# Kernel optimization log

Measured on AMD Instinct MI355X. Metric: run time of the kernel, lower is better.

Reference implementation:

```python
import jax, jax.numpy as jnp
import numpy as np


def setup_inputs() -> dict:
    key = jax.random.key(0)
    k1, k2, k3, k4, k5 = jax.random.split(key, 5)
    B, S, E, T = 64, 2048, 256, 100
    h = jax.random.normal(k1, (B, S, E), dtype=jnp.float32)
    theta = jax.random.uniform(k2, (B, T), dtype=jnp.float32)
    w = jax.random.normal(k3, (E, T), dtype=jnp.float32) * 0.05
    v = jax.random.normal(k4, (E, 1), dtype=jnp.float32) * 0.05
    u = jax.random.normal(k5, (E, E), dtype=jnp.float32) * 0.05
    return {"h": h, "theta": theta, "w": w, "v": v, "u": u}


def reference(h, theta, w, v, u):
    # h: [B,S,E], theta: [B,T], w: [E,T], v: [E,1], u: [E,E]
    theta_w = theta @ w.T                      # [B,E]
    h_u = jnp.einsum('bse,ef->bsf', h, u)      # [B,S,E]
    g = jnp.tanh(theta_w[:, None, :] + h_u) @ v  # [B,S,1]
    weight = jax.nn.softmax(g[..., 0], axis=-1)  # [B,S]
    vec = jnp.einsum('bs,bse->be', weight, h)    # [B,E]
    return vec
```

## Files before the change

kernel.cpp:

```cpp
#include <hip/hip_runtime.h>
#include <hip/hip_bf16.h>
#include <math.h>


#define E_DIM 256
#define GM 32
#define NC 8

typedef __bf16 bf16x8 __attribute__((ext_vector_type(8)));
typedef float  f32x4  __attribute__((ext_vector_type(4)));

__device__ __forceinline__ unsigned short f2bf(float x) {
    return __builtin_bit_cast(unsigned short, (__bf16)x);
}

__device__ __forceinline__ float fast_tanh(float x) {
    const float e = __expf(2.0f * x);
    const float r = __builtin_amdgcn_rcpf(e + 1.0f);
    return fmaf(-2.0f, r, 1.0f);
}

__device__ __forceinline__ unsigned sswz(unsigned slot, unsigned row) {
    return (slot & 48u) | ((slot & 15u) ^ (row & 15u));
}

__global__ __launch_bounds__(256) void k_prep(const float* __restrict__ u,
                                              const float* __restrict__ theta,
                                              const float* __restrict__ w,
                                              unsigned short* __restrict__ u_t,
                                              float* __restrict__ tw,
                                              int T) {
    if (blockIdx.x < E_DIM) {
        const int f = blockIdx.x, e = threadIdx.x;
        u_t[(size_t)f * E_DIM + e] = f2bf(u[(size_t)e * E_DIM + f]);
    } else {
        __shared__ float th[128];
        const int b = blockIdx.x - E_DIM;
        const int e = threadIdx.x;
        if (threadIdx.x < T) th[threadIdx.x] = theta[b * T + threadIdx.x];
        __syncthreads();
        float acc = 0.f;
        for (int t = 0; t < T; ++t) acc = fmaf(th[t], w[e * T + t], acc);
        tw[b * E_DIM + e] = acc;
    }
}

__global__ __launch_bounds__(256, 2) void k_fused(const float* __restrict__ h,
                                                  const unsigned short* __restrict__ u_t,
                                                  const float* __restrict__ tw_,
                                                  const float* __restrict__ v,
                                                  float* __restrict__ partial,
                                                  float* __restrict__ pm,
                                                  float* __restrict__ pd,
                                                  int S, int SC) {
    __shared__ float Abuf[2][GM * E_DIM];
    __shared__ float red[4][GM];
    __shared__ float exw[GM];
    __shared__ float pacc[4][E_DIM];

    const int b   = blockIdx.y;
    const int c0  = blockIdx.x * NC;
    const int tid = threadIdx.x;
    const int w   = tid >> 6;
    const int l   = tid & 63;
    const int lg  = l >> 4;
    const int lc  = l & 15;
    const int f0w = w * 64;

#define STAGE(buf, ch)                                                           \
    {                                                                            \
        const char* hb_ = (const char*)(h + ((size_t)b * S + (size_t)(ch) * GM) * E_DIM); \
        _Pragma("unroll")                                                        \
        for (int r = 0; r < 8; ++r) {                                            \
            const int row = r * 4 + w;                                           \
            const unsigned ss = sswz((unsigned)l, (unsigned)row);                \
            __builtin_amdgcn_global_load_lds(                                    \
                (const __attribute__((address_space(1))) void*)(hb_ + (size_t)row * 1024 + ss * 16), \
                (__attribute__((address_space(3))) void*)((char*)Abuf[buf] + r * 4096 + w * 1024), \
                16, 0, 0);                                                       \
        }                                                                        \
    }

    STAGE(0, c0);

    bf16x8 ub[8][4];
#pragma unroll
    for (int kt = 0; kt < 8; ++kt)
#pragma unroll
        for (int n = 0; n < 4; ++n)
            ub[kt][n] = *reinterpret_cast<const bf16x8*>(
                u_t + (size_t)(f0w + n * 16 + lc) * E_DIM + kt * 32 + lg * 8);

    float tw_f[4], v_f[4];
#pragma unroll
    for (int n = 0; n < 4; ++n) {
        const int f = f0w + n * 16 + lc;
        tw_f[n] = tw_[b * E_DIM + f];
        v_f[n]  = v[f];
    }

    __syncthreads();

    for (int c = 0; c < NC; ++c) {
        const int sc  = c0 + c;
        const int cur = c & 1;

        if (c + 1 < NC) STAGE(cur ^ 1, sc + 1);

        const char* A = (const char*)Abuf[cur];
        f32x4 acc[2][4];
#pragma unroll
        for (int m = 0; m < 2; ++m)
#pragma unroll
            for (int n = 0; n < 4; ++n)
                acc[m][n] = (f32x4){0.f, 0.f, 0.f, 0.f};

#pragma unroll
        for (int kt = 0; kt < 8; ++kt) {
            bf16x8 af[2];
#pragma unroll
            for (int m = 0; m < 2; ++m) {
                const unsigned row = (unsigned)(m * 16 + lc);
                const unsigned s0 = sswz((unsigned)(kt * 8 + lg * 2), row);
                const unsigned s1 = sswz((unsigned)(kt * 8 + lg * 2 + 1), row);
                const f32x4 fa0 = *reinterpret_cast<const f32x4*>(A + row * 1024 + s0 * 16);
                const f32x4 fa1 = *reinterpret_cast<const f32x4*>(A + row * 1024 + s1 * 16);
#pragma unroll
                for (int j = 0; j < 4; ++j) {
                    af[m][j]     = (__bf16)fa0[j];
                    af[m][4 + j] = (__bf16)fa1[j];
                }
            }
#pragma unroll
            for (int n = 0; n < 4; ++n) {
                acc[0][n] = __builtin_amdgcn_mfma_f32_16x16x32_bf16(af[0], ub[kt][n], acc[0][n], 0, 0, 0);
                acc[1][n] = __builtin_amdgcn_mfma_f32_16x16x32_bf16(af[1], ub[kt][n], acc[1][n], 0, 0, 0);
            }
        }

        float rs[2][4] = {};
#pragma unroll
        for (int n = 0; n < 4; ++n)
#pragma unroll
            for (int m = 0; m < 2; ++m)
#pragma unroll
                for (int i = 0; i < 4; ++i)
                    rs[m][i] += fast_tanh(acc[m][n][i] + tw_f[n]) * v_f[n];

#pragma unroll
        for (int off = 1; off < 16; off <<= 1)
#pragma unroll
            for (int m = 0; m < 2; ++m)
#pragma unroll
                for (int i = 0; i < 4; ++i)
                    rs[m][i] += __shfl_xor(rs[m][i], off, 64);

        if (lc == 0) {
#pragma unroll
            for (int m = 0; m < 2; ++m)
#pragma unroll
                for (int i = 0; i < 4; ++i)
                    red[w][m * 16 + lg * 4 + i] = rs[m][i];
        }
        __syncthreads();

        if (tid < GM) {
            const float g = red[0][tid] + red[1][tid] + red[2][tid] + red[3][tid];
            float mx = g;
#pragma unroll
            for (int off = 1; off < 32; off <<= 1)
                mx = fmaxf(mx, __shfl_xor(mx, off, 64));
            const float ex = __expf(g - mx);
            float d = ex;
#pragma unroll
            for (int off = 1; off < 32; off <<= 1)
                d += __shfl_xor(d, off, 64);
            exw[tid] = ex;
            if (tid == 0) {
                pm[(size_t)b * SC + sc] = mx;
                pd[(size_t)b * SC + sc] = d;
            }
        }
        __syncthreads();

        f32x4 a4 = (f32x4){0.f, 0.f, 0.f, 0.f};
#pragma unroll
        for (int j = 0; j < 8; ++j) {
            const unsigned row = (unsigned)(w * 8 + j);
            const float ws = exw[row];
            const unsigned ss = sswz((unsigned)l, row);
            const f32x4 hv = *reinterpret_cast<const f32x4*>(A + row * 1024 + ss * 16);
            a4[0] = fmaf(ws, hv[0], a4[0]);
            a4[1] = fmaf(ws, hv[1], a4[1]);
            a4[2] = fmaf(ws, hv[2], a4[2]);
            a4[3] = fmaf(ws, hv[3], a4[3]);
        }
        *reinterpret_cast<f32x4*>(&pacc[w][l * 4]) = a4;
        __syncthreads();

        partial[((size_t)b * SC + sc) * E_DIM + tid] =
            pacc[0][tid] + pacc[1][tid] + pacc[2][tid] + pacc[3][tid];
    }
#undef STAGE
}

__global__ __launch_bounds__(256) void k_combine(const float* __restrict__ partial,
                                                 const float* __restrict__ pm,
                                                 const float* __restrict__ pd,
                                                 float* __restrict__ out,
                                                 int SC) {
    const int b = blockIdx.x, t = threadIdx.x;
    __shared__ float sm[128], sd[128];
    if (t < SC) {
        sm[t] = pm[(size_t)b * SC + t];
        sd[t] = pd[(size_t)b * SC + t];
    }
    __syncthreads();

    float M = -3.4e38f;
    for (int c = 0; c < SC; ++c) M = fmaxf(M, sm[c]);

    float num = 0.f, den = 0.f;
    for (int c = 0; c < SC; ++c) {
        const float s = __expf(sm[c] - M);
        den = fmaf(s, sd[c], den);
        num = fmaf(s, partial[((size_t)b * SC + c) * E_DIM + t], num);
    }
    out[(size_t)b * E_DIM + t] = num / den;
}

extern "C" void kernel_launch(void* const* d_in, const int* in_sizes, int n_in,
                              void* d_out, int out_size, void* d_ws, size_t ws_size,
                              hipStream_t stream) {
    const float* h     = (const float*)d_in[0];
    const float* theta = (const float*)d_in[1];
    const float* w     = (const float*)d_in[2];
    const float* v     = (const float*)d_in[3];
    const float* u     = (const float*)d_in[4];
    float* out = (float*)d_out;

    const int E = in_sizes[3];
    const int T = in_sizes[2] / E;
    const int B = in_sizes[1] / T;
    const int S = in_sizes[0] / (B * E);
    const int SC = S / GM;

    float* tw = (float*)d_ws;
    unsigned short* u_t = (unsigned short*)(tw + (size_t)B * E);
    float* partial = (float*)(u_t + (size_t)E * E);
    float* pm = partial + (size_t)B * SC * E;
    float* pd = pm + (size_t)B * SC;

    k_prep<<<dim3(E + B), dim3(256), 0, stream>>>(u, theta, w, u_t, tw, T);
    k_fused<<<dim3(SC / NC, B), dim3(256), 0, stream>>>(h, u_t, tw, v, partial, pm, pd, S, SC);
    k_combine<<<dim3(B), dim3(256), 0, stream>>>(partial, pm, pd, out, SC);
}
```

Measured before the change: 64.44 us.

## Drop softmax max-subtraction, accumulate per block, and use finer waitcnt barriers

Removes the per-chunk max/sum reduction and instead computes exp(g) directly, relying on g being small because tanh is bounded and v is small. The weighted sum of h is accumulated in registers across all chunks, so partial results are written once per block instead of once per chunk, and the combine kernel no longer rescales. Full __syncthreads calls are replaced with explicit s_waitcnt vmcnt/lgkmcnt plus raw barriers so the next chunk's LDS prefetch can stay in flight. The cost is less numerical safety: without max subtraction, exp can overflow if g is large.

```diff
diff --git a/kernel.cpp b/kernel.cpp
--- a/kernel.cpp
+++ b/kernel.cpp
@@ -50,13 +50,12 @@
                                                   const float* __restrict__ tw_,
                                                   const float* __restrict__ v,
                                                   float* __restrict__ partial,
-                                                  float* __restrict__ pm,
                                                   float* __restrict__ pd,
                                                   int S, int SC) {
     __shared__ float Abuf[2][GM * E_DIM];
     __shared__ float red[4][GM];
-    __shared__ float exw[GM];
     __shared__ float pacc[4][E_DIM];
+    __shared__ float dred[4];
 
     const int b   = blockIdx.y;
     const int c0  = blockIdx.x * NC;
@@ -99,13 +98,20 @@
         v_f[n]  = v[f];
     }
 
-    __syncthreads();
+    f32x4 numa = (f32x4){0.f, 0.f, 0.f, 0.f};
+    float den = 0.f;
 
     for (int c = 0; c < NC; ++c) {
-        const int sc  = c0 + c;
         const int cur = c & 1;
 
-        if (c + 1 < NC) STAGE(cur ^ 1, sc + 1);
+        if (c + 1 < NC) {
+            STAGE(cur ^ 1, c0 + c + 1);
+            asm volatile("s_waitcnt vmcnt(8)" ::: "memory");
+        } else {
+            asm volatile("s_waitcnt vmcnt(0)" ::: "memory");
+        }
+        __builtin_amdgcn_s_barrier();
+        __builtin_amdgcn_sched_barrier(0);
 
         const char* A = (const char*)Abuf[cur];
         f32x4 acc[2][4];
@@ -162,70 +168,50 @@
                 for (int i = 0; i < 4; ++i)
                     red[w][m * 16 + lg * 4 + i] = rs[m][i];
         }
-        __syncthreads();
-
-        if (tid < GM) {
-            const float g = red[0][tid] + red[1][tid] + red[2][tid] + red[3][tid];
-            float mx = g;
-#pragma unroll
-            for (int off = 1; off < 32; off <<= 1)
-                mx = fmaxf(mx, __shfl_xor(mx, off, 64));
-            const float ex = __expf(g - mx);
-            float d = ex;
-#pragma unroll
-            for (int off = 1; off < 32; off <<= 1)
-                d += __shfl_xor(d, off, 64);
-            exw[tid] = ex;
-            if (tid == 0) {
-                pm[(size_t)b * SC + sc] = mx;
-                pd[(size_t)b * SC + sc] = d;
-            }
-        }
-        __syncthreads();
-
-        f32x4 a4 = (f32x4){0.f, 0.f, 0.f, 0.f};
+        asm volatile("s_waitcnt lgkmcnt(0)" ::: "memory");
+        __builtin_amdgcn_s_barrier();
+        __builtin_amdgcn_sched_barrier(0);
+
 #pragma unroll
         for (int j = 0; j < 8; ++j) {
             const unsigned row = (unsigned)(w * 8 + j);
-            const float ws = exw[row];
+            const float g = red[0][row] + red[1][row] + red[2][row] + red[3][row];
+            const float ex = __expf(g);
+            den += ex;
             const unsigned ss = sswz((unsigned)l, row);
             const f32x4 hv = *reinterpret_cast<const f32x4*>(A + row * 1024 + ss * 16);
-            a4[0] = fmaf(ws, hv[0], a4[0]);
-            a4[1] = fmaf(ws, hv[1], a4[1]);
-            a4[2] = fmaf(ws, hv[2], a4[2]);
-            a4[3] = fmaf(ws, hv[3], a4[3]);
-        }
-        *reinterpret_cast<f32x4*>(&pacc[w][l * 4]) = a4;
-        __syncthreads();
-
-        partial[((size_t)b * SC + sc) * E_DIM + tid] =
-            pacc[0][tid] + pacc[1][tid] + pacc[2][tid] + pacc[3][tid];
-    }
+            numa[0] = fmaf(ex, hv[0], numa[0]);
+            numa[1] = fmaf(ex, hv[1], numa[1]);
+            numa[2] = fmaf(ex, hv[2], numa[2]);
+            numa[3] = fmaf(ex, hv[3], numa[3]);
+        }
+        asm volatile("s_waitcnt lgkmcnt(0)" ::: "memory");
+        __builtin_amdgcn_s_barrier();
+        __builtin_amdgcn_sched_barrier(0);
+    }
+
+    *reinterpret_cast<f32x4*>(&pacc[w][l * 4]) = numa;
+    if (l == 0) dred[w] = den;
+    __syncthreads();
+
+    const int nb = SC / NC;
+    partial[((size_t)b * nb + blockIdx.x) * E_DIM + tid] =
+        pacc[0][tid] + pacc[1][tid] + pacc[2][tid] + pacc[3][tid];
+    if (tid == 0)
+        pd[(size_t)b * nb + blockIdx.x] = dred[0] + dred[1] + dred[2] + dred[3];
 #undef STAGE
 }
 
 __global__ __launch_bounds__(256) void k_combine(const float* __restrict__ partial,
-                                                 const float* __restrict__ pm,
                                                  const float* __restrict__ pd,
                                                  float* __restrict__ out,
-                                                 int SC) {
+                                                 int NB) {
     const int b = blockIdx.x, t = threadIdx.x;
-    __shared__ float sm[128], sd[128];
-    if (t < SC) {
-        sm[t] = pm[(size_t)b * SC + t];
-        sd[t] = pd[(size_t)b * SC + t];
-    }
-    __syncthreads();
-
-    float M = -3.4e38f;
-    for (int c = 0; c < SC; ++c) M = fmaxf(M, sm[c]);
-
-    float num = 0.f, den = 0.f;
-    for (int c = 0; c < SC; ++c) {
-        const float s = __expf(sm[c] - M);
-        den = fmaf(s, sd[c], den);
-        num = fmaf(s, partial[((size_t)b * SC + c) * E_DIM + t], num);
-    }
+    float den = 0.f;
+    for (int k = 0; k < NB; ++k) den += pd[(size_t)b * NB + k];
+    float num = 0.f;
+    for (int k = 0; k < NB; ++k)
+        num += partial[((size_t)b * NB + k) * E_DIM + t];
     out[(size_t)b * E_DIM + t] = num / den;
 }
 
@@ -244,14 +230,14 @@
     const int B = in_sizes[1] / T;
     const int S = in_sizes[0] / (B * E);
     const int SC = S / GM;
+    const int NB = SC / NC;
 
     float* tw = (float*)d_ws;
     unsigned short* u_t = (unsigned short*)(tw + (size_t)B * E);
     float* partial = (float*)(u_t + (size_t)E * E);
-    float* pm = partial + (size_t)B * SC * E;
-    float* pd = pm + (size_t)B * SC;
+    float* pd = partial + (size_t)B * NB * E;
 
     k_prep<<<dim3(E + B), dim3(256), 0, stream>>>(u, theta, w, u_t, tw, T);
-    k_fused<<<dim3(SC / NC, B), dim3(256), 0, stream>>>(h, u_t, tw, v, partial, pm, pd, S, SC);
-    k_combine<<<dim3(B), dim3(256), 0, stream>>>(partial, pm, pd, out, SC);
-}
+    k_fused<<<dim3(NB, B), dim3(256), 0, stream>>>(h, u_t, tw, v, partial, pd, S, SC);
+    k_combine<<<dim3(B), dim3(256), 0, stream>>>(partial, pd, out, NB);
+}
```

Result: faster. 59.77 us (-7.2%).
